# Optimization experiments

Hardware: AMD Instinct MI355X
Metric: run time of the kernel (lower is better)

## Reference

```python
import jax, jax.numpy as jnp
import numpy as np

H = 16
DK = 64


def setup_inputs() -> dict:
    key = jax.random.key(0)
    ks = jax.random.split(key, 10)
    dps, seq_len, d = 32, 2048, 1024
    xavier = float(np.sqrt(2.0 / (DK + DK)))  # xavier_normal_ for square dk x dk
    return {
        "S": jax.random.normal(ks[0], (dps, seq_len, d), dtype=jnp.float32),
        "R": jax.random.normal(ks[1], (dps, 1, d), dtype=jnp.float32),
        "S_mas": jax.random.randint(ks[2], (dps, seq_len, 1), 0, 2, dtype=jnp.int32),
        "R_mas": jax.random.randint(ks[3], (dps, 1, 1), 0, 2, dtype=jnp.int32),
        "WQ_w": jax.random.normal(ks[4], (DK, DK), dtype=jnp.float32) * xavier,
        "WQ_b": jnp.zeros((DK,), dtype=jnp.float32),
        "WK_w": jax.random.normal(ks[5], (DK, DK), dtype=jnp.float32) * xavier,
        "WK_b": jnp.zeros((DK,), dtype=jnp.float32),
        "WV_w": jax.random.normal(ks[6], (DK, DK), dtype=jnp.float32) * xavier,
        "WV_b": jnp.zeros((DK,), dtype=jnp.float32),
    }


def reference(S, R, S_mas, R_mas, WQ_w, WQ_b, WK_w, WK_b, WV_w, WV_b):
    dps, seq_len, d = S.shape
    # split heads: (dps, seq, h, dk) -- permute-free since projections are per last dim
    S4 = S.reshape(dps, seq_len, H, DK)
    R4 = R.reshape(dps, 1, H, DK)
    # only S_Q, R_K, R_V affect the output (S_K, S_V, R_Q are dead in the original)
    S_Q = jnp.einsum("bshd,ed->bshe", S4, WQ_w) + WQ_b
    R_K = jnp.einsum("bshd,ed->bshe", R4, WK_w) + WK_b  # (dps,1,h,dk)
    R_V = jnp.einsum("bshd,ed->bshe", R4, WV_w) + WV_b  # (dps,1,h,dk)
    # dot-product gate per (batch, token, head)
    beta = jnp.sum(S_Q * R_K, axis=-1, keepdims=True)  # (dps,seq,h,1)
    S_Z = R_V * beta                                   # (dps,seq,h,dk)
    mask = (S_mas != 0)[:, :, :, None]                 # (dps,seq,1,1)
    S_Z = jnp.where(mask, S_Z, 0.0)
    return S_Z.reshape(dps, seq_len, H * DK)
```

## Files before the change

kernel.cpp:

```cpp
#include <hip/hip_runtime.h>

#define H 16
#define DK 64

typedef float vfloat4 __attribute__((ext_vector_type(4)));

__global__ __launch_bounds__(64) void prep_kernel(
    const float* __restrict__ R,
    const float* __restrict__ WQ_w, const float* __restrict__ WQ_b,
    const float* __restrict__ WK_w, const float* __restrict__ WK_b,
    const float* __restrict__ WV_w, const float* __restrict__ WV_b,
    float* __restrict__ u, float* __restrict__ rv, float* __restrict__ c) {
    const int bh = blockIdx.x;
    const int e  = threadIdx.x;
    __shared__ float r_s[DK];
    __shared__ float rk_s[DK];

    r_s[e] = R[bh * DK + e];
    __syncthreads();

    float rk  = WK_b[e];
    float rvv = WV_b[e];
#pragma unroll
    for (int d = 0; d < DK; ++d) {
        rk  += r_s[d] * WK_w[e * DK + d];
        rvv += r_s[d] * WV_w[e * DK + d];
    }
    rk_s[e] = rk;
    rv[bh * DK + e] = rvv;
    __syncthreads();

    float uu = 0.f;
#pragma unroll
    for (int ee = 0; ee < DK; ++ee) uu += WQ_w[ee * DK + e] * rk_s[ee];
    u[bh * DK + e] = uu;

    if (e == 0) {
        float cc = 0.f;
        for (int ee = 0; ee < DK; ++ee) cc += WQ_b[ee] * rk_s[ee];
        c[bh] = cc;
    }
}

#define ROWS_PER_BLOCK 16

__global__ __launch_bounds__(256) void fused_kernel(
    const float* __restrict__ S, const int* __restrict__ S_mas,
    const float* __restrict__ u, const float* __restrict__ rv,
    const float* __restrict__ c, float* __restrict__ out,
    int seq_len, int blocks_per_batch) {
    const int t = threadIdx.x;
    const int h = t >> 4;
    const int b = blockIdx.x / blocks_per_batch;
    const int srow0 = (blockIdx.x % blocks_per_batch) * ROWS_PER_BLOCK;
    const int d_model = H * DK;

    const int bh = b * H + h;
    const vfloat4 u4  = *(const vfloat4*)(u  + bh * DK + (t & 15) * 4);
    const vfloat4 rv4 = *(const vfloat4*)(rv + bh * DK + (t & 15) * 4);
    const float   ch  = c[bh];

    const size_t base = (size_t)b * seq_len * d_model + (size_t)srow0 * d_model + t * 4;
    const float* srow = S + base;
    float*       orow = out + base;
    const int*   mrow = S_mas + (size_t)b * seq_len + srow0;

    int m[ROWS_PER_BLOCK];
#pragma unroll
    for (int r = 0; r < ROWS_PER_BLOCK; ++r) m[r] = mrow[r];

    vfloat4 sdat[ROWS_PER_BLOCK];
#pragma unroll
    for (int r = 0; r < ROWS_PER_BLOCK; ++r) {
        const size_t off = (m[r] != 0) ? (size_t)r * d_model : 0;
        sdat[r] = *(const vfloat4*)(srow + off);
    }

#pragma unroll
    for (int r = 0; r < ROWS_PER_BLOCK; ++r) {
        const vfloat4 s4 = sdat[r];
        float p = s4.x * u4.x + s4.y * u4.y + s4.z * u4.z + s4.w * u4.w;
        p += __shfl_xor(p, 1);
        p += __shfl_xor(p, 2);
        p += __shfl_xor(p, 4);
        p += __shfl_xor(p, 8);
        const float beta = p + ch;
        const bool live = (m[r] != 0);
        vfloat4 o4;
        o4.x = live ? rv4.x * beta : 0.f;
        o4.y = live ? rv4.y * beta : 0.f;
        o4.z = live ? rv4.z * beta : 0.f;
        o4.w = live ? rv4.w * beta : 0.f;
        *(vfloat4*)(orow + (size_t)r * d_model) = o4;
    }
}

extern "C" void kernel_launch(void* const* d_in, const int* in_sizes, int n_in,
                              void* d_out, int out_size, void* d_ws, size_t ws_size,
                              hipStream_t stream) {
    const float* S     = (const float*)d_in[0];
    const float* R     = (const float*)d_in[1];
    const int*   S_mas = (const int*)d_in[2];
    const float* WQ_w  = (const float*)d_in[4];
    const float* WQ_b  = (const float*)d_in[5];
    const float* WK_w  = (const float*)d_in[6];
    const float* WK_b  = (const float*)d_in[7];
    const float* WV_w  = (const float*)d_in[8];
    const float* WV_b  = (const float*)d_in[9];
    float* out = (float*)d_out;

    const int d_model = H * DK;
    const int dps     = in_sizes[1] / d_model;
    const int seq_len = in_sizes[0] / (dps * d_model);

    float* u_ws  = (float*)d_ws;
    float* rv_ws = u_ws + (size_t)dps * H * DK;
    float* c_ws  = rv_ws + (size_t)dps * H * DK;

    prep_kernel<<<dps * H, 64, 0, stream>>>(R, WQ_w, WQ_b, WK_w, WK_b, WV_w, WV_b,
                                            u_ws, rv_ws, c_ws);

    const int blocks_per_batch = seq_len / ROWS_PER_BLOCK;
    fused_kernel<<<dps * blocks_per_batch, 256, 0, stream>>>(
        S, S_mas, u_ws, rv_ws, c_ws, out, seq_len, blocks_per_batch);
}
```

Before: 425.2 us.

## Split fused gate kernel into separate beta-compute and output-expand kernels

```diff
diff --git a/kernel.cpp b/kernel.cpp
--- a/kernel.cpp
+++ b/kernel.cpp
@@ -4,6 +4,7 @@
 #define DK 64
 
 typedef float vfloat4 __attribute__((ext_vector_type(4)));
+
 
 __global__ __launch_bounds__(64) void prep_kernel(
     const float* __restrict__ R,
@@ -44,11 +45,10 @@
 
 #define ROWS_PER_BLOCK 16
 
-__global__ __launch_bounds__(256) void fused_kernel(
+__global__ __launch_bounds__(256) void gate_kernel(
     const float* __restrict__ S, const int* __restrict__ S_mas,
-    const float* __restrict__ u, const float* __restrict__ rv,
-    const float* __restrict__ c, float* __restrict__ out,
-    int seq_len, int blocks_per_batch) {
+    const float* __restrict__ u, const float* __restrict__ c,
+    float* __restrict__ beta, int seq_len, int blocks_per_batch) {
     const int t = threadIdx.x;
     const int h = t >> 4;
     const int b = blockIdx.x / blocks_per_batch;
@@ -56,13 +56,11 @@
     const int d_model = H * DK;
 
     const int bh = b * H + h;
-    const vfloat4 u4  = *(const vfloat4*)(u  + bh * DK + (t & 15) * 4);
-    const vfloat4 rv4 = *(const vfloat4*)(rv + bh * DK + (t & 15) * 4);
-    const float   ch  = c[bh];
+    const vfloat4 u4 = *(const vfloat4*)(u + bh * DK + (t & 15) * 4);
+    const float  ch  = c[bh];
 
     const size_t base = (size_t)b * seq_len * d_model + (size_t)srow0 * d_model + t * 4;
     const float* srow = S + base;
-    float*       orow = out + base;
     const int*   mrow = S_mas + (size_t)b * seq_len + srow0;
 
     int m[ROWS_PER_BLOCK];
@@ -76,6 +74,7 @@
         sdat[r] = *(const vfloat4*)(srow + off);
     }
 
+    float* brow = beta + ((size_t)b * seq_len + srow0) * H + h;
 #pragma unroll
     for (int r = 0; r < ROWS_PER_BLOCK; ++r) {
         const vfloat4 s4 = sdat[r];
@@ -84,13 +83,34 @@
         p += __shfl_xor(p, 2);
         p += __shfl_xor(p, 4);
         p += __shfl_xor(p, 8);
-        const float beta = p + ch;
-        const bool live = (m[r] != 0);
+        const float bv = (m[r] != 0) ? (p + ch) : 0.f;
+        if ((t & 15) == 0) brow[(size_t)r * H] = bv;
+    }
+}
+
+__global__ __launch_bounds__(256) void expand_kernel(
+    const float* __restrict__ rv, const float* __restrict__ beta,
+    float* __restrict__ out, int seq_len, int blocks_per_batch) {
+    const int t = threadIdx.x;
+    const int h = t >> 4;
+    const int b = blockIdx.x / blocks_per_batch;
+    const int srow0 = (blockIdx.x % blocks_per_batch) * ROWS_PER_BLOCK;
+    const int d_model = H * DK;
+
+    const int bh = b * H + h;
+    const vfloat4 rv4 = *(const vfloat4*)(rv + bh * DK + (t & 15) * 4);
+
+    const float* brow = beta + ((size_t)b * seq_len + srow0) * H + h;
+    float bt[ROWS_PER_BLOCK];
+#pragma unroll
+    for (int r = 0; r < ROWS_PER_BLOCK; ++r) bt[r] = brow[(size_t)r * H];
+
+    float* orow = out + (size_t)b * seq_len * d_model + (size_t)srow0 * d_model + t * 4;
+#pragma unroll
+    for (int r = 0; r < ROWS_PER_BLOCK; ++r) {
         vfloat4 o4;
-        o4.x = live ? rv4.x * beta : 0.f;
-        o4.y = live ? rv4.y * beta : 0.f;
-        o4.z = live ? rv4.z * beta : 0.f;
-        o4.w = live ? rv4.w * beta : 0.f;
+        o4.x = rv4.x * bt[r]; o4.y = rv4.y * bt[r];
+        o4.z = rv4.z * bt[r]; o4.w = rv4.w * bt[r];
         *(vfloat4*)(orow + (size_t)r * d_model) = o4;
     }
 }
@@ -113,14 +133,17 @@
     const int dps     = in_sizes[1] / d_model;
     const int seq_len = in_sizes[0] / (dps * d_model);
 
-    float* u_ws  = (float*)d_ws;
-    float* rv_ws = u_ws + (size_t)dps * H * DK;
-    float* c_ws  = rv_ws + (size_t)dps * H * DK;
+    float* u_ws    = (float*)d_ws;
+    float* rv_ws   = u_ws + (size_t)dps * H * DK;
+    float* c_ws    = rv_ws + (size_t)dps * H * DK;
+    float* beta_ws = c_ws + (size_t)dps * H;
 
     prep_kernel<<<dps * H, 64, 0, stream>>>(R, WQ_w, WQ_b, WK_w, WK_b, WV_w, WV_b,
                                             u_ws, rv_ws, c_ws);
 
     const int blocks_per_batch = seq_len / ROWS_PER_BLOCK;
-    fused_kernel<<<dps * blocks_per_batch, 256, 0, stream>>>(
-        S, S_mas, u_ws, rv_ws, c_ws, out, seq_len, blocks_per_batch);
+    gate_kernel<<<dps * blocks_per_batch, 256, 0, stream>>>(
+        S, S_mas, u_ws, c_ws, beta_ws, seq_len, blocks_per_batch);
+    expand_kernel<<<dps * blocks_per_batch, 256, 0, stream>>>(
+        rv_ws, beta_ws, out, seq_len, blocks_per_batch);
 }
```

Result: slower. 444.9 us (+4.6%).
